# Performance work log

Hardware: AMD Instinct MI355X
Metric: run time of the kernel (lower is better)

## Reference

```python
import jax, jax.numpy as jnp
import numpy as np
import math

B, N, DIM = 8, 4096, 768
H, D = 12, 64
STAGES = 3
LN_EPS = 1e-5

def _ln(x, g, b):
    mu = jnp.mean(x, axis=-1, keepdims=True)
    var = jnp.mean(jnp.square(x - mu), axis=-1, keepdims=True)
    return (x - mu) * jax.lax.rsqrt(var + LN_EPS) * g + b

def _mlp(x, W, b, g, be):
    return jax.nn.gelu(_ln(x @ W + b, g, be), approximate=False)

def setup_inputs() -> dict:
    key = jax.random.key(0)
    ks = jax.random.split(key, 16)
    s = lambda i, shape, sc: jax.random.normal(ks[i], shape, jnp.float32) * sc
    return {
        "x": s(0, (B, N, DIM), 1.0),
        "Wq": s(1, (DIM, H * D), DIM ** -0.5),
        "Wk": s(2, (DIM, H * D), DIM ** -0.5),
        "Wv": s(3, (DIM, H * D), DIM ** -0.5),
        "pool_W": s(4, (STAGES, D, D), D ** -0.5),
        "pool_b": jnp.zeros((STAGES, D), jnp.float32),
        "pool_g": jnp.ones((STAGES, D), jnp.float32),
        "pool_be": jnp.zeros((STAGES, D), jnp.float32),
        "exp_W": s(5, (STAGES, D, D), D ** -0.5),
        "exp_b": jnp.zeros((STAGES, D), jnp.float32),
        "exp_g": jnp.ones((STAGES, D), jnp.float32),
        "exp_be": jnp.zeros((STAGES, D), jnp.float32),
        "Wo": s(6, (H * D, DIM), (H * D) ** -0.5),
        "bo": jnp.zeros((DIM,), jnp.float32),
    }

def reference(x, Wq, Wk, Wv, pool_W, pool_b, pool_g, pool_be,
              exp_W, exp_b, exp_g, exp_be, Wo, bo):
    b, n, _ = x.shape
    # project and split heads -> (b, h, n, d)
    def heads(y):
        return y.reshape(b, n, H, D).transpose(0, 2, 1, 3)
    q = heads(x @ Wq)
    k = heads(x @ Wk)
    v = heads(x @ Wv)
    fmap = lambda t: jax.nn.elu(t) + 1.0
    q = fmap(q)
    k = fmap(k)

    kc, vc = k, v
    for i in range(STAGES):
        s = kc.shape[2]
        if s > 1:
            pad = (-s) % 2
            if pad:
                kc = jnp.pad(kc, ((0, 0), (0, 0), (0, pad), (0, 0)))
                vc = jnp.pad(vc, ((0, 0), (0, 0), (0, pad), (0, 0)))
            kc = kc.reshape(b, H, -1, 2, D).mean(axis=3)
            kc = _mlp(kc, pool_W[i], pool_b[i], pool_g[i], pool_be[i])
            vc = vc.reshape(b, H, -1, 2, D).mean(axis=3)

    kc = kc / math.sqrt(kc.shape[2])
    kv = jnp.einsum('bhnd,bhne->bhde', kc, vc)       # (b,h,d,d)
    out = jnp.einsum('bhnd,bhde->bhne', q, kv)       # (b,h,n,d)
    k_sum = kc.sum(axis=2, keepdims=True)            # (b,h,1,d)
    q_k_sum = jnp.sum(q * k_sum, axis=-1, keepdims=True)  # (b,h,n,1)
    out = out / (q_k_sum + 1e-6)

    for i in reversed(range(STAGES)):
        out = _mlp(out, exp_W[i], exp_b[i], exp_g[i], exp_be[i])

    out = out.transpose(0, 2, 1, 3).reshape(b, n, H * D)
    return out @ Wo + bo
```

## Files before the change

### kernel.cpp

```cpp
#include <hip/hip_runtime.h>
#include <math.h>

#define B_   8
#define N_   4096
#define DIM_ 768
#define H_   12
#define D_   64

typedef unsigned short ushort_t;
typedef unsigned int uint_t;
typedef __attribute__((ext_vector_type(8))) short short8;
typedef __attribute__((ext_vector_type(4))) float f32x4;

__device__ __forceinline__ float gelu_exact(float z) {
  const float ax = fabsf(z) * 0.70710678118654752440f;
  const float t  = __builtin_amdgcn_rcpf(1.f + 0.3275911f * ax);
  float poly = ((((1.061405429f * t - 1.453152027f) * t + 1.421413741f) * t
                 - 0.284496736f) * t + 0.254829592f) * t;
  const float erfax = 1.f - poly * __expf(-ax * ax);
  const float erfv = __builtin_copysignf(erfax, z);
  return 0.5f * z * (1.f + erfv);
}

__device__ __forceinline__ ushort_t f2bf(float f) {
  union { float f; unsigned u; } x; x.f = f;
  unsigned r = x.u + 0x7FFFu + ((x.u >> 16) & 1u);
  return (ushort_t)(r >> 16);
}

__device__ __forceinline__ float bf2f(ushort_t h) {
  union { unsigned u; float f; } x; x.u = ((unsigned)h) << 16;
  return x.f;
}

__device__ __forceinline__ void gl_lds16(const ushort_t* g, ushort_t* l) {
  __builtin_amdgcn_global_load_lds(
      (const __attribute__((address_space(1))) void*)g,
      (__attribute__((address_space(3))) void*)l, 16, 0, 0);
}

__global__ __launch_bounds__(256) void transpose_w_bf16(
    const float* __restrict__ src, ushort_t* __restrict__ dst)
{
  __shared__ float t[32][33];
  const int lx = threadIdx.x & 31, ly = threadIdx.x >> 5;
  const int bx = blockIdx.x * 32;
  const int by = blockIdx.y * 32;
  #pragma unroll
  for (int j = 0; j < 32; j += 8)
    t[ly + j][lx] = src[(size_t)(by + ly + j) * 768 + bx + lx];
  __syncthreads();
  #pragma unroll
  for (int j = 0; j < 32; j += 8)
    dst[(size_t)(bx + ly + j) * 768 + by + lx] = f2bf(t[lx][ly + j]);
}

__global__ __launch_bounds__(256) void transpose64_bf16(
    const float* __restrict__ pW, const float* __restrict__ eW,
    ushort_t* __restrict__ dst)
{
  const int m = blockIdx.x;
  const float* src = (m < 3) ? (pW + m * 4096) : (eW + (m - 3) * 4096);
  ushort_t* o = dst + m * 4096;
  for (int i = threadIdx.x; i < 4096; i += 256) {
    const int r = i >> 6, c = i & 63;
    o[c * 64 + r] = f2bf(src[r * 64 + c]);
  }
}

__global__ __launch_bounds__(192) void conv_pool8(
    const float* __restrict__ src, ushort_t* __restrict__ dst,
    ushort_t* __restrict__ x8)
{
  const int g = blockIdx.x;
  const int t = threadIdx.x;
  const float4* s = (const float4*)(src + (size_t)g * 8 * 768);
  ushort4* d = (ushort4*)(dst + (size_t)g * 8 * 768);
  float4 sum = {0.f, 0.f, 0.f, 0.f};
  #pragma unroll
  for (int j = 0; j < 8; ++j) {
    float4 f = s[j * 192 + t];
    ushort4 o;
    o.x = f2bf(f.x); o.y = f2bf(f.y); o.z = f2bf(f.z); o.w = f2bf(f.w);
    d[j * 192 + t] = o;
    sum.x += f.x; sum.y += f.y; sum.z += f.z; sum.w += f.w;
  }
  ushort4 m;
  m.x = f2bf(0.125f * sum.x); m.y = f2bf(0.125f * sum.y);
  m.z = f2bf(0.125f * sum.z); m.w = f2bf(0.125f * sum.w);
  ((ushort4*)(x8 + (size_t)g * 768))[t] = m;
}

#define GEMM_MAINLOOP(A, Bt, K)                                               \
  __shared__ ushort_t As[128 * 64];                                           \
  __shared__ ushort_t Bs[128 * 64];                                           \
  const int tid = threadIdx.x;                                                \
  const int nwg_ = (int)(gridDim.x * gridDim.y);                              \
  const int wgid0_ = (int)(blockIdx.y * gridDim.x + blockIdx.x);              \
  const int wgid_ = (wgid0_ & 7) * (nwg_ >> 3) + (wgid0_ >> 3);               \
  const int row0 = (wgid_ / (int)gridDim.x) * 128;                            \
  const int col0 = (wgid_ % (int)gridDim.x) * 128;                            \
  const ushort_t* pA[4]; const ushort_t* pB[4];                               \
  _Pragma("unroll")                                                           \
  for (int j = 0; j < 4; ++j) {                                               \
    const int g_ = tid + j * 256;                                             \
    const int rr = g_ >> 3, sc = g_ & 7;                                      \
    pA[j] = (A) + (size_t)(row0 + rr) * (K) + ((sc ^ (rr & 7)) << 3);         \
    pB[j] = (Bt) + (size_t)(col0 + rr) * (K) + ((sc ^ (rr & 7)) << 3);        \
  }                                                                           \
  const int w = tid >> 6, lane = tid & 63;                                    \
  const int stw = w * 512;                                                    \
  const int wm = w >> 1, wn = w & 1;                                          \
  const int qd = lane >> 4, l15 = lane & 15;                                  \
  const int s0 = ((qd ^ (l15 & 7)) << 3);                                     \
  const int abase = (wm * 64 + l15) * 64;                                     \
  const int bbase = (wn * 64 + l15) * 64;                                     \
  f32x4 acc[4][4] = {};                                                       \
  for (int k0 = 0; k0 < (K); k0 += 64) {                                      \
    __syncthreads();                                                          \
    _Pragma("unroll")                                                         \
    for (int j = 0; j < 4; ++j) gl_lds16(pA[j] + k0, As + j * 2048 + stw);    \
    _Pragma("unroll")                                                         \
    for (int j = 0; j < 4; ++j) gl_lds16(pB[j] + k0, Bs + j * 2048 + stw);    \
    __syncthreads();                                                          \
    short8 af[4], bfr[4];                                                     \
    _Pragma("unroll")                                                         \
    for (int mt = 0; mt < 4; ++mt) af[mt] = *(const short8*)&As[abase + mt * 1024 + s0]; \
    _Pragma("unroll")                                                         \
    for (int nt = 0; nt < 4; ++nt) bfr[nt] = *(const short8*)&Bs[bbase + nt * 1024 + s0]; \
    _Pragma("unroll")                                                         \
    for (int mt = 0; mt < 4; ++mt)                                            \
      _Pragma("unroll")                                                       \
      for (int nt = 0; nt < 4; ++nt)                                          \
        acc[mt][nt] = __builtin_amdgcn_mfma_f32_16x16x32_bf16(                \
            af[mt], bfr[nt], acc[mt][nt], 0, 0, 0);                           \
    _Pragma("unroll")                                                         \
    for (int mt = 0; mt < 4; ++mt) af[mt] = *(const short8*)&As[abase + mt * 1024 + (s0 ^ 32)]; \
    _Pragma("unroll")                                                         \
    for (int nt = 0; nt < 4; ++nt) bfr[nt] = *(const short8*)&Bs[bbase + nt * 1024 + (s0 ^ 32)]; \
    _Pragma("unroll")                                                         \
    for (int mt = 0; mt < 4; ++mt)                                            \
      _Pragma("unroll")                                                       \
      for (int nt = 0; nt < 4; ++nt)                                          \
        acc[mt][nt] = __builtin_amdgcn_mfma_f32_16x16x32_bf16(                \
            af[mt], bfr[nt], acc[mt][nt], 0, 0, 0);                           \
  }

__global__ __launch_bounds__(256) void gemm_qkv(
    const ushort_t* __restrict__ A, const ushort_t* __restrict__ Bt,
    ushort_t* __restrict__ qo, ushort_t* __restrict__ ko)
{
  GEMM_MAINLOOP(A, Bt, 768)
  const int sel = col0 / 768;
  const int colbase = (col0 % 768) + wn * 64;
  ushort_t* o = (sel == 0) ? qo : ko;
  #pragma unroll
  for (int mt = 0; mt < 4; ++mt) {
    #pragma unroll
    for (int nt = 0; nt < 4; ++nt) {
      const int cg = colbase + nt * 16 + l15;
      #pragma unroll
      for (int r = 0; r < 4; ++r) {
        const int rg = row0 + wm * 64 + mt * 16 + qd * 4 + r;
        const float vv = acc[mt][nt][r];
        const float e = (vv > 0.f) ? vv + 1.f : __expf(vv);
        o[(size_t)rg * 768 + cg] = f2bf(e);
      }
    }
  }
}

__global__ __launch_bounds__(256) void gemm_v(
    const ushort_t* __restrict__ A, const ushort_t* __restrict__ Bt,
    float* __restrict__ vco)
{
  GEMM_MAINLOOP(A, Bt, 768)
  #pragma unroll
  for (int mt = 0; mt < 4; ++mt) {
    #pragma unroll
    for (int nt = 0; nt < 4; ++nt) {
      const int cg = col0 + wn * 64 + nt * 16 + l15;
      const int hh = cg >> 6, d = cg & 63;
      #pragma unroll
      for (int r = 0; r < 4; ++r) {
        const int rg = row0 + wm * 64 + mt * 16 + qd * 4 + r;
        const int b = rg >> 9, n = rg & 511;
        vco[(((size_t)b * 12 + hh) * 512 + n) * 64 + d] = acc[mt][nt][r];
      }
    }
  }
}

__global__ __launch_bounds__(256) void gemm_out(
    const ushort_t* __restrict__ A, const ushort_t* __restrict__ Bt,
    const float* __restrict__ bo, float* __restrict__ C)
{
  GEMM_MAINLOOP(A, Bt, 768)
  #pragma unroll
  for (int mt = 0; mt < 4; ++mt) {
    #pragma unroll
    for (int nt = 0; nt < 4; ++nt) {
      const int cg = col0 + wn * 64 + nt * 16 + l15;
      #pragma unroll
      for (int r = 0; r < 4; ++r) {
        const int rg = row0 + wm * 64 + mt * 16 + qd * 4 + r;
        C[(size_t)rg * 768 + cg] = acc[mt][nt][r] + bo[cg];
      }
    }
  }
}

__device__ __forceinline__ void mlp_stage(
    const ushort_t* __restrict__ inb, ushort_t* __restrict__ outb,
    const ushort_t* __restrict__ Wls, const float* __restrict__ bias,
    const float* __restrict__ g, const float* __restrict__ be,
    int rowbase, int ntiles, int tid)
{
  if (ntiles == 0) return;
  const int lane = tid & 63, quad = lane >> 4, l15 = lane & 15;
  float bv[4], gv[4], bev[4];
  #pragma unroll
  for (int nt = 0; nt < 4; ++nt) {
    const int c = nt * 16 + l15;
    bv[nt] = bias[c]; gv[nt] = g[c]; bev[nt] = be[c];
  }
  f32x4 a2[2][4];
  #pragma unroll
  for (int mt = 0; mt < 2; ++mt)
    #pragma unroll
    for (int nt = 0; nt < 4; ++nt)
      a2[mt][nt] = f32x4{bv[nt], bv[nt], bv[nt], bv[nt]};

  #pragma unroll
  for (int ks = 0; ks < 2; ++ks) {
    short8 af[2], bfr[4];
    #pragma unroll
    for (int mt = 0; mt < 2; ++mt)
      if (mt < ntiles)
        af[mt] = *(const short8*)&inb[(rowbase + mt * 16 + l15) * 72 + ks * 32 + quad * 8];
    #pragma unroll
    for (int nt = 0; nt < 4; ++nt)
      bfr[nt] = *(const short8*)&Wls[(nt * 16 + l15) * 72 + ks * 32 + quad * 8];
    #pragma unroll
    for (int mt = 0; mt < 2; ++mt)
      if (mt < ntiles)
        #pragma unroll
        for (int nt = 0; nt < 4; ++nt)
          a2[mt][nt] = __builtin_amdgcn_mfma_f32_16x16x32_bf16(af[mt], bfr[nt], a2[mt][nt], 0, 0, 0);
  }

  #pragma unroll
  for (int mt = 0; mt < 2; ++mt) {
    if (mt >= ntiles) continue;
    #pragma unroll
    for (int r = 0; r < 4; ++r) {
      float sum = a2[mt][0][r] + a2[mt][1][r] + a2[mt][2][r] + a2[mt][3][r];
      #pragma unroll
      for (int m = 1; m < 16; m <<= 1) sum += __shfl_xor(sum, m, 64);
      const float mu = sum * 0.015625f;
      float dv[4], var = 0.f;
      #pragma unroll
      for (int nt = 0; nt < 4; ++nt) { dv[nt] = a2[mt][nt][r] - mu; var += dv[nt] * dv[nt]; }
      #pragma unroll
      for (int m = 1; m < 16; m <<= 1) var += __shfl_xor(var, m, 64);
      const float rstd = rsqrtf(var * 0.015625f + 1e-5f);
      const int rl = rowbase + mt * 16 + quad * 4 + r;
      #pragma unroll
      for (int nt = 0; nt < 4; ++nt) {
        const float z = dv[nt] * rstd * gv[nt] + bev[nt];
        outb[rl * 72 + nt * 16 + l15] = f2bf(gelu_exact(z));
      }
    }
  }
}

__device__ __forceinline__ void pool_pairs(
    const ushort_t* __restrict__ inb, ushort_t* __restrict__ outb,
    int outRows, int tid)
{
  for (int idx = tid; idx < outRows * 8; idx += 256) {
    const int rl = idx >> 3, ch = idx & 7;
    short8 a = *(const short8*)&inb[(2 * rl) * 72 + ch * 8];
    short8 b = *(const short8*)&inb[(2 * rl + 1) * 72 + ch * 8];
    short8 o;
    #pragma unroll
    for (int e = 0; e < 8; ++e)
      o[e] = (short)f2bf(0.5f * (bf2f((ushort_t)a[e]) + bf2f((ushort_t)b[e])));
    *(short8*)&outb[rl * 72 + ch * 8] = o;
  }
}

__global__ __launch_bounds__(256) void pool_kv_fused(
    const ushort_t* __restrict__ k16, const float* __restrict__ vc,
    const ushort_t* __restrict__ pWt,
    const float* __restrict__ pb, const float* __restrict__ pg,
    const float* __restrict__ pbe,
    float* __restrict__ kvp, float* __restrict__ ksp)
{
  __shared__ ushort_t Wl[3 * 64 * 72];
  __shared__ ushort_t bufA[128 * 72];
  __shared__ ushort_t bufB[128 * 72];
  __shared__ float    vs[32 * 64];
  const int tid = threadIdx.x;
  const int x = blockIdx.x;
  const int h = blockIdx.y;
  const int bb = blockIdx.z;
  const ushort_t* kin = k16 + (size_t)bb * 3145728;
  const float* vp = vc + (size_t)bb * 393216 + ((size_t)h * 512 + x * 32) * 64;

  {
    const uint_t* ws = (const uint_t*)pWt;
    for (int i = tid; i < 6144; i += 256) {
      const int s = i >> 11, rem = i & 2047, r = rem >> 5, c = rem & 31;
      ((uint_t*)(Wl + (s * 64 + r) * 72))[c] = ws[i];
    }
  }
  #pragma unroll
  for (int j = 0; j < 4; ++j) {
    const int idx = j * 256 + tid;
    const int rl = idx >> 3, ch = idx & 7;
    const ushort_t* p = kin + (size_t)h * 64 + (size_t)(2 * (x * 128 + rl)) * 768 + ch * 8;
    short8 a = *(const short8*)p;
    short8 b2 = *(const short8*)(p + 768);
    short8 o;
    #pragma unroll
    for (int e = 0; e < 8; ++e)
      o[e] = (short)f2bf(0.5f * (bf2f((ushort_t)a[e]) + bf2f((ushort_t)b2[e])));
    *(short8*)&bufA[rl * 72 + ch * 8] = o;
  }
  #pragma unroll
  for (int i = 0; i < 2; ++i)
    ((float4*)vs)[tid + 256 * i] = ((const float4*)vp)[tid + 256 * i];
  __syncthreads();

  const int w = tid >> 6;
  mlp_stage(bufA, bufB, Wl, pb, pg, pbe, w * 32, 2, tid);
  __syncthreads();
  pool_pairs(bufB, bufA, 64, tid);
  __syncthreads();
  mlp_stage(bufA, bufB, Wl + 64 * 72, pb + 64, pg + 64, pbe + 64, w * 16, 1, tid);
  __syncthreads();
  pool_pairs(bufB, bufA, 32, tid);
  __syncthreads();
  mlp_stage(bufA, bufB, Wl + 128 * 72, pb + 128, pg + 128, pbe + 128,
            w * 16, (w < 2) ? 1 : 0, tid);
  __syncthreads();

  const int e = tid & 63;
  const int dg = tid >> 6;
  float acc[16] = {};
  float accs = 0.f;
  for (int nn = 0; nn < 32; ++nn) {
    const float vv = vs[nn * 64 + e];
    #pragma unroll
    for (int j = 0; j < 16; ++j)
      acc[j] += bf2f(bufB[nn * 72 + dg * 16 + j]) * vv;
    if (tid < 64) accs += bf2f(bufB[nn * 72 + tid]);
  }
  float* o = kvp + (size_t)bb * 786432 + ((size_t)h * 16 + x) * 4096;
  #pragma unroll
  for (int j = 0; j < 16; ++j)
    o[(dg * 16 + j) * 64 + e] = acc[j];
  if (tid < 64) ksp[(size_t)bb * 12288 + (h * 16 + x) * 64 + tid] = accs;
}

__global__ __launch_bounds__(256) void kv_reduce_t(
    const float* __restrict__ kvp, const float* __restrict__ ksp,
    ushort_t* __restrict__ kvxT)
{
  const int bb = blockIdx.y;
  kvp  += (size_t)bb * 786432;
  ksp  += (size_t)bb * 12288;
  kvxT += (size_t)bb * 61440;
  const int idx = blockIdx.x * 256 + threadIdx.x;
  const int h = idx / 5120;
  const int rem = idx - h * 5120;
  const int er = rem >> 6, d = rem & 63;
  const float scale = 0.044194173824159216f;
  float val = 0.f;
  if (er < 64) {
    float s = 0.f;
    #pragma unroll
    for (int c = 0; c < 16; ++c) s += kvp[((size_t)h * 16 + c) * 4096 + d * 64 + er];
    val = s * scale;
  } else if (er == 64) {
    float s = 0.f;
    #pragma unroll
    for (int c = 0; c < 16; ++c) s += ksp[(h * 16 + c) * 64 + d];
    val = s * scale;
  }
  kvxT[idx] = f2bf(val);
}

__global__ __launch_bounds__(256) void attn_exp_mfma(
    const ushort_t* __restrict__ q16, const ushort_t* __restrict__ kvxT,
    const ushort_t* __restrict__ eWt,
    const float* __restrict__ eb, const float* __restrict__ eg,
    const float* __restrict__ ebe, ushort_t* __restrict__ out16)
{
  __shared__ ushort_t Wl[3 * 64 * 72];
  __shared__ ushort_t tl[128 * 72];
  const int tid = threadIdx.x;
  const int h = blockIdx.y;
  const int bb = blockIdx.z;
  const int row0 = blockIdx.x * 128;
  q16   += (size_t)bb * 3145728;
  out16 += (size_t)bb * 3145728;
  const ushort_t* kvx = kvxT + (size_t)bb * 61440 + (size_t)h * 5120;

  {
    const uint_t* ws = (const uint_t*)eWt;
    for (int i = tid; i < 6144; i += 256) {
      const int s = i >> 11, rem = i & 2047, r = rem >> 5, c = rem & 31;
      ((uint_t*)(Wl + (s * 64 + r) * 72))[c] = ws[i];
    }
  }
  __syncthreads();

  const int w = tid >> 6, lane = tid & 63;
  const int quad = lane >> 4, l15 = lane & 15;

  f32x4 acc[2][5] = {};
  #pragma unroll
  for (int ks = 0; ks < 2; ++ks) {
    short8 af[2], bfr[5];
    #pragma unroll
    for (int mt = 0; mt < 2; ++mt) {
      const int rg = row0 + w * 32 + mt * 16 + l15;
      af[mt] = *(const short8*)(q16 + (size_t)rg * 768 + h * 64 + ks * 32 + quad * 8);
    }
    #pragma unroll
    for (int nt = 0; nt < 5; ++nt)
      bfr[nt] = *(const short8*)(kvx + (nt * 16 + l15) * 64 + ks * 32 + quad * 8);
    #pragma unroll
    for (int mt = 0; mt < 2; ++mt)
      #pragma unroll
      for (int nt = 0; nt < 5; ++nt)
        acc[mt][nt] = __builtin_amdgcn_mfma_f32_16x16x32_bf16(af[mt], bfr[nt], acc[mt][nt], 0, 0, 0);
  }

  float t[2][4][4];
  #pragma unroll
  for (int mt = 0; mt < 2; ++mt)
    #pragma unroll
    for (int r = 0; r < 4; ++r) {
      const float den = __shfl(acc[mt][4][r], lane & 48, 64) + 1e-6f;
      const float inv = __builtin_amdgcn_rcpf(den);
      #pragma unroll
      for (int nt = 0; nt < 4; ++nt)
        t[mt][nt][r] = acc[mt][nt][r] * inv;
    }

  for (int s = 2; s >= 0; --s) {
    __syncthreads();
    #pragma unroll
    for (int mt = 0; mt < 2; ++mt)
      #pragma unroll
      for (int nt = 0; nt < 4; ++nt)
        #pragma unroll
        for (int r = 0; r < 4; ++r)
          tl[(w * 32 + mt * 16 + quad * 4 + r) * 72 + nt * 16 + l15] = f2bf(t[mt][nt][r]);
    __syncthreads();

    float bv[4], gv[4], bev[4];
    #pragma unroll
    for (int nt = 0; nt < 4; ++nt) {
      const int c = s * 64 + nt * 16 + l15;
      bv[nt] = eb[c]; gv[nt] = eg[c]; bev[nt] = ebe[c];
    }
    f32x4 a2[2][4];
    #pragma unroll
    for (int mt = 0; mt < 2; ++mt)
      #pragma unroll
      for (int nt = 0; nt < 4; ++nt)
        a2[mt][nt] = f32x4{bv[nt], bv[nt], bv[nt], bv[nt]};

    #pragma unroll
    for (int ks = 0; ks < 2; ++ks) {
      short8 af[2], bfr[4];
      #pragma unroll
      for (int mt = 0; mt < 2; ++mt)
        af[mt] = *(const short8*)&tl[(w * 32 + mt * 16 + l15) * 72 + ks * 32 + quad * 8];
      #pragma unroll
      for (int nt = 0; nt < 4; ++nt)
        bfr[nt] = *(const short8*)&Wl[(s * 64 + nt * 16 + l15) * 72 + ks * 32 + quad * 8];
      #pragma unroll
      for (int mt = 0; mt < 2; ++mt)
        #pragma unroll
        for (int nt = 0; nt < 4; ++nt)
          a2[mt][nt] = __builtin_amdgcn_mfma_f32_16x16x32_bf16(af[mt], bfr[nt], a2[mt][nt], 0, 0, 0);
    }

    #pragma unroll
    for (int mt = 0; mt < 2; ++mt)
      #pragma unroll
      for (int r = 0; r < 4; ++r) {
        float sum = a2[mt][0][r] + a2[mt][1][r] + a2[mt][2][r] + a2[mt][3][r];
        #pragma unroll
        for (int m = 1; m < 16; m <<= 1) sum += __shfl_xor(sum, m, 64);
        const float mu = sum * 0.015625f;
        float dv[4], var = 0.f;
        #pragma unroll
        for (int nt = 0; nt < 4; ++nt) { dv[nt] = a2[mt][nt][r] - mu; var += dv[nt] * dv[nt]; }
        #pragma unroll
        for (int m = 1; m < 16; m <<= 1) var += __shfl_xor(var, m, 64);
        const float rstd = rsqrtf(var * 0.015625f + 1e-5f);
        #pragma unroll
        for (int nt = 0; nt < 4; ++nt) {
          const float z = dv[nt] * rstd * gv[nt] + bev[nt];
          t[mt][nt][r] = gelu_exact(z);
        }
      }
  }

  #pragma unroll
  for (int mt = 0; mt < 2; ++mt)
    #pragma unroll
    for (int nt = 0; nt < 4; ++nt)
      #pragma unroll
      for (int r = 0; r < 4; ++r) {
        const int rg = row0 + w * 32 + mt * 16 + quad * 4 + r;
        out16[(size_t)rg * 768 + h * 64 + nt * 16 + l15] = f2bf(t[mt][nt][r]);
      }
}

extern "C" void kernel_launch(void* const* d_in, const int* in_sizes, int n_in,
                              void* d_out, int out_size, void* d_ws, size_t ws_size,
                              hipStream_t stream)
{
  const float* x   = (const float*)d_in[0];
  const float* Wq  = (const float*)d_in[1];
  const float* Wk  = (const float*)d_in[2];
  const float* Wv  = (const float*)d_in[3];
  const float* pW  = (const float*)d_in[4];
  const float* pb  = (const float*)d_in[5];
  const float* pg  = (const float*)d_in[6];
  const float* pbe = (const float*)d_in[7];
  const float* eW  = (const float*)d_in[8];
  const float* eb  = (const float*)d_in[9];
  const float* eg  = (const float*)d_in[10];
  const float* ebe = (const float*)d_in[11];
  const float* Wo  = (const float*)d_in[12];
  const float* bo  = (const float*)d_in[13];
  float* outp = (float*)d_out;

  unsigned char* wsb = (unsigned char*)d_ws;
  ushort_t* WqkvT = (ushort_t*)(wsb + 0);
  ushort_t* WoT   = (ushort_t*)(wsb + 3538944);
  ushort_t* Wt6   = (ushort_t*)(wsb + 4718592);
  const size_t CB   = 4767744;
  const size_t PERB = 26861568;

  int NB;
  if      (ws_size >= CB + 8 * PERB) NB = 8;
  else if (ws_size >= CB + 4 * PERB) NB = 4;
  else if (ws_size >= CB + 2 * PERB) NB = 2;
  else if (ws_size >= CB + 1 * PERB) NB = 1;
  else return;

  unsigned char* cb = wsb + CB;
  ushort_t* xb16 = (ushort_t*)(cb);
  ushort_t* q16  = (ushort_t*)(cb + (size_t)NB *  6291456);
  ushort_t* k16  = (ushort_t*)(cb + (size_t)NB * 12582912);
  float*    vc   = (float*)   (cb + (size_t)NB * 18874368);
  ushort_t* kc_a = (ushort_t*)(cb + (size_t)NB * 20447232);
  ushort_t* kc_b = (ushort_t*)(cb + (size_t)NB * 23592960);
  ushort_t* kvxT = (ushort_t*)(cb + (size_t)NB * 25952256);
  ushort_t* x8   = (ushort_t*)(cb + (size_t)NB * 26075136);
  float* kvp = (float*)kc_a;
  float* ksp = (float*)kc_b;
  ushort_t* ao16 = xb16;

  const ushort_t* pWt = Wt6;
  const ushort_t* eWt = Wt6 + 3 * 4096;
  const size_t SB = (size_t)N_ * DIM_;

  transpose_w_bf16<<<dim3(24, 24), 256, 0, stream>>>(Wq, WqkvT);
  transpose_w_bf16<<<dim3(24, 24), 256, 0, stream>>>(Wk, WqkvT + 768 * 768);
  transpose_w_bf16<<<dim3(24, 24), 256, 0, stream>>>(Wv, WqkvT + 2 * 768 * 768);
  transpose_w_bf16<<<dim3(24, 24), 256, 0, stream>>>(Wo, WoT);
  transpose64_bf16<<<6, 256, 0, stream>>>(pW, eW, Wt6);

  const ushort_t* WvT = WqkvT + 2 * 768 * 768;

  for (int b0 = 0; b0 < B_; b0 += NB) {
    const float* xc = x + (size_t)b0 * SB;
    float* oc = outp + (size_t)b0 * SB;

    conv_pool8<<<NB * 512, 192, 0, stream>>>(xc, xb16, x8);
    gemm_qkv<<<dim3(12, NB * 32), 256, 0, stream>>>(xb16, WqkvT, q16, k16);
    gemm_v<<<dim3(6, NB * 4), 256, 0, stream>>>(x8, WvT, vc);

    pool_kv_fused<<<dim3(16, 12, NB), 256, 0, stream>>>(k16, vc, pWt,
                                                        pb, pg, pbe, kvp, ksp);
    kv_reduce_t<<<dim3(240, NB), 256, 0, stream>>>(kvp, ksp, kvxT);

    attn_exp_mfma<<<dim3(32, 12, NB), 256, 0, stream>>>(q16, kvxT, eWt,
                                                        eb, eg, ebe, ao16);

    gemm_out<<<dim3(6, NB * 32), 256, 0, stream>>>(ao16, WoT, bo, oc);
  }
}
```

Baseline: 566.6 us.

## Double-buffer GEMM mainloop LDS tiles with prefetch two stages ahead

Doubles the shared-memory A/B tiles and turns the GEMM mainloop into a two-stage pipeline. Global-to-LDS loads for tile k+2 are issued while tile k is computed, gated by explicit vmcnt waits and raw s_barrier. The aim is to hide global load latency behind MFMA work. In exchange LDS use doubles to 64KB per block, which may lower occupancy. The hand-written waitcnt/barrier ordering also risks subtle races if the LDS writes are not fully waited on before a barrier.

```diff
diff --git a/kernel.cpp b/kernel.cpp
--- a/kernel.cpp
+++ b/kernel.cpp
@@ -91,9 +91,27 @@
   ((ushort4*)(x8 + (size_t)g * 768))[t] = m;
 }
 
+#define GEMM_STAGE(kk, bofs)                                                  \
+    _Pragma("unroll")                                                         \
+    for (int j = 0; j < 4; ++j) gl_lds16(pA[j] + (kk) * 64, As + (bofs) + j * 2048 + stw); \
+    _Pragma("unroll")                                                         \
+    for (int j = 0; j < 4; ++j) gl_lds16(pB[j] + (kk) * 64, Bs + (bofs) + j * 2048 + stw);
+
+#define GEMM_COMPUTE_HALF(bofs, soff)                                         \
+    _Pragma("unroll")                                                         \
+    for (int mt = 0; mt < 4; ++mt) af[mt] = *(const short8*)&As[(bofs) + abase + mt * 1024 + (soff)]; \
+    _Pragma("unroll")                                                         \
+    for (int nt = 0; nt < 4; ++nt) bfr[nt] = *(const short8*)&Bs[(bofs) + bbase + nt * 1024 + (soff)]; \
+    _Pragma("unroll")                                                         \
+    for (int mt = 0; mt < 4; ++mt)                                            \
+      _Pragma("unroll")                                                       \
+      for (int nt = 0; nt < 4; ++nt)                                          \
+        acc[mt][nt] = __builtin_amdgcn_mfma_f32_16x16x32_bf16(                \
+            af[mt], bfr[nt], acc[mt][nt], 0, 0, 0);
+
 #define GEMM_MAINLOOP(A, Bt, K)                                               \
-  __shared__ ushort_t As[128 * 64];                                           \
-  __shared__ ushort_t Bs[128 * 64];                                           \
+  __shared__ ushort_t As[2 * 128 * 64];                                       \
+  __shared__ ushort_t Bs[2 * 128 * 64];                                       \
   const int tid = threadIdx.x;                                                \
   const int nwg_ = (int)(gridDim.x * gridDim.y);                              \
   const int wgid0_ = (int)(blockIdx.y * gridDim.x + blockIdx.x);              \
@@ -116,34 +134,21 @@
   const int abase = (wm * 64 + l15) * 64;                                     \
   const int bbase = (wn * 64 + l15) * 64;                                     \
   f32x4 acc[4][4] = {};                                                       \
-  for (int k0 = 0; k0 < (K); k0 += 64) {                                      \
-    __syncthreads();                                                          \
-    _Pragma("unroll")                                                         \
-    for (int j = 0; j < 4; ++j) gl_lds16(pA[j] + k0, As + j * 2048 + stw);    \
-    _Pragma("unroll")                                                         \
-    for (int j = 0; j < 4; ++j) gl_lds16(pB[j] + k0, Bs + j * 2048 + stw);    \
-    __syncthreads();                                                          \
-    short8 af[4], bfr[4];                                                     \
-    _Pragma("unroll")                                                         \
-    for (int mt = 0; mt < 4; ++mt) af[mt] = *(const short8*)&As[abase + mt * 1024 + s0]; \
-    _Pragma("unroll")                                                         \
-    for (int nt = 0; nt < 4; ++nt) bfr[nt] = *(const short8*)&Bs[bbase + nt * 1024 + s0]; \
-    _Pragma("unroll")                                                         \
-    for (int mt = 0; mt < 4; ++mt)                                            \
-      _Pragma("unroll")                                                       \
-      for (int nt = 0; nt < 4; ++nt)                                          \
-        acc[mt][nt] = __builtin_amdgcn_mfma_f32_16x16x32_bf16(                \
-            af[mt], bfr[nt], acc[mt][nt], 0, 0, 0);                           \
-    _Pragma("unroll")                                                         \
-    for (int mt = 0; mt < 4; ++mt) af[mt] = *(const short8*)&As[abase + mt * 1024 + (s0 ^ 32)]; \
-    _Pragma("unroll")                                                         \
-    for (int nt = 0; nt < 4; ++nt) bfr[nt] = *(const short8*)&Bs[bbase + nt * 1024 + (s0 ^ 32)]; \
-    _Pragma("unroll")                                                         \
-    for (int mt = 0; mt < 4; ++mt)                                            \
-      _Pragma("unroll")                                                       \
-      for (int nt = 0; nt < 4; ++nt)                                          \
-        acc[mt][nt] = __builtin_amdgcn_mfma_f32_16x16x32_bf16(                \
-            af[mt], bfr[nt], acc[mt][nt], 0, 0, 0);                           \
+  const int NT_ = (K) / 64;                                                   \
+  GEMM_STAGE(0, 0)                                                            \
+  GEMM_STAGE(1, 8192)                                                         \
+  for (int kt = 0; kt < NT_; ++kt) {                                          \
+    const int bo_ = (kt & 1) * 8192;                                          \
+    if (kt < NT_ - 1) { asm volatile("s_waitcnt vmcnt(8)" ::: "memory"); }    \
+    else              { asm volatile("s_waitcnt vmcnt(0)" ::: "memory"); }    \
+    asm volatile("s_barrier" ::: "memory");                                   \
+    {                                                                         \
+      short8 af[4], bfr[4];                                                   \
+      GEMM_COMPUTE_HALF(bo_, s0)                                              \
+      GEMM_COMPUTE_HALF(bo_, (s0 ^ 32))                                       \
+    }                                                                         \
+    asm volatile("s_barrier" ::: "memory");                                   \
+    if (kt + 2 < NT_) { GEMM_STAGE(kt + 2, bo_) }                             \
   }
 
 __global__ __launch_bounds__(256) void gemm_qkv(
```

Result: slower. 608.9 us (+7.5%).
